# Optimization experiments

Hardware: AMD Instinct MI355X
Metric: run time of the kernel (lower is better)

Reference implementation:

```python
import jax, jax.numpy as jnp
import numpy as np

IN_DIM = 1024
LOW_D_FF = 128
OUT_DIM = 1024
B = 8
S = 2048

def _xavier_normal(key, shape):
    fan_in, fan_out = shape[1], shape[0]
    std = float(np.sqrt(2.0 / (fan_in + fan_out)))
    return jax.random.normal(key, shape, dtype=jnp.float32) * std

def setup_inputs() -> dict:
    key = jax.random.key(0)
    kx, kk, kd, ku = jax.random.split(key, 4)
    x = jax.random.normal(kx, (B, S, IN_DIM), dtype=jnp.float32)
    k = jax.random.normal(kk, (B, LOW_D_FF), dtype=jnp.float32)
    D_matrix = _xavier_normal(kd, (IN_DIM * LOW_D_FF, LOW_D_FF))
    U_matrix = _xavier_normal(ku, (LOW_D_FF * OUT_DIM, LOW_D_FF))
    return {"x": x, "k": k, "D_matrix": D_matrix, "U_matrix": U_matrix}

def reference(x, k, D_matrix, U_matrix):
    # x: [B, S, in_dim], k: [B, low_d_ff]
    Bn = x.shape[0]
    low = k.shape[-1]
    # hypernetwork weight generation: per-sample D [B, in_dim, low], U [B, low, out_dim]
    D = jnp.einsum('pk,bk->bp', D_matrix, k).reshape(Bn, IN_DIM, low)
    U = jnp.einsum('pk,bk->bp', U_matrix, k).reshape(Bn, low, OUT_DIM)
    h = jax.nn.relu(jnp.einsum('bsd,bdl->bsl', x, D))
    return jnp.einsum('bsl,blo->bso', h, U)
```

## Files before the change

### kernel.cpp

```cpp
#include <hip/hip_runtime.h>
#include <hip/hip_bf16.h>
#include <stdint.h>

#define IN_DIM  1024
#define LOW     128
#define OUT_DIM 1024
#define BATCH   8
#define SEQ     2048

typedef unsigned short u16;
typedef short bf16x8 __attribute__((ext_vector_type(8)));
typedef unsigned short u16x4 __attribute__((ext_vector_type(4)));
typedef float f32x4 __attribute__((ext_vector_type(4)));

__device__ __forceinline__ u16 f2bf(float f) {
    union { float f; uint32_t u; } v;
    v.f = f;
    uint32_t u = v.u;
    return (u16)((u + 0x7fffu + ((u >> 16) & 1u)) >> 16);
}

__global__ __launch_bounds__(256) void gen_w(const float* __restrict__ Dm,
                                             const float* __restrict__ Um,
                                             const float* __restrict__ kv,
                                             u16* __restrict__ DgT,
                                             u16* __restrict__ UgT) {
    __shared__ u16 tb[8 * 8 * 32];

    int t = threadIdx.x;
    int bid = blockIdx.x;
    bool isU = bid >= 512;
    int rb = isU ? (bid - 512) : bid;
    const float* src = isU ? Um : Dm;
    u16* outp = isU ? UgT : DgT;
    int NTOT = isU ? 1024 : 128;
    int MTOT = isU ? 128 : 1024;
    int sh = isU ? 7 : 4;
    int m0 = (rb >> sh) * 32;
    int n0 = (rb & ((1 << sh) - 1)) * 8;

    int lane = t & 63, w = t >> 6;
    int lr = lane & 15;
    int hi = lane >> 4;

    bf16x8 bfrag[4];
#pragma unroll
    for (int ks = 0; ks < 4; ++ks)
#pragma unroll
        for (int j = 0; j < 8; ++j) {
            float kvf = (lr < 8) ? kv[lr * LOW + ks * 32 + hi * 8 + j] : 0.f;
            bfrag[ks][j] = (short)f2bf(kvf);
        }

    const float* abase = src +
        ((size_t)(m0 + w * 8 + (lr >> 3)) * NTOT + n0 + (lr & 7)) * 128 + hi * 8;
    size_t tstep = (size_t)2 * NTOT * 128;

#define ISSUE(Lb, tau)                                                        \
    {                                                                         \
        const float* rp = abase + (size_t)(tau) * tstep;                      \
        _Pragma("unroll")                                                     \
        for (int ks = 0; ks < 4; ++ks) {                                      \
            Lb[2 * ks]     = *(const f32x4*)(rp + ks * 32);                   \
            Lb[2 * ks + 1] = *(const f32x4*)(rp + ks * 32 + 4);               \
        }                                                                     \
    }

#define COMPUTE(Lb, tau)                                                      \
    {                                                                         \
        f32x4 acc = (f32x4){0.f, 0.f, 0.f, 0.f};                              \
        _Pragma("unroll")                                                     \
        for (int ks = 0; ks < 4; ++ks) {                                      \
            f32x4 v0 = Lb[2 * ks], v1 = Lb[2 * ks + 1];                       \
            bf16x8 afr;                                                       \
            afr[0] = (short)f2bf(v0.x); afr[1] = (short)f2bf(v0.y);           \
            afr[2] = (short)f2bf(v0.z); afr[3] = (short)f2bf(v0.w);           \
            afr[4] = (short)f2bf(v1.x); afr[5] = (short)f2bf(v1.y);           \
            afr[6] = (short)f2bf(v1.z); afr[7] = (short)f2bf(v1.w);           \
            acc = __builtin_amdgcn_mfma_f32_16x16x32_bf16(afr, bfrag[ks],     \
                                                          acc, 0, 0, 0);      \
        }                                                                     \
        if (lr < 8) {                                                         \
            _Pragma("unroll")                                                 \
            for (int j = 0; j < 4; ++j) {                                     \
                int r = hi * 4 + j;                                           \
                int mm = w * 8 + (tau) * 2 + (r >> 3);                        \
                tb[lr * 256 + (r & 7) * 32 + mm] = f2bf(acc[j]);              \
            }                                                                 \
        }                                                                     \
    }

    f32x4 LA[8], LB[8];
    ISSUE(LA, 0)
    ISSUE(LB, 1)
    COMPUTE(LA, 0)
    ISSUE(LA, 2)
    COMPUTE(LB, 1)
    ISSUE(LB, 3)
    COMPUTE(LA, 2)
    COMPUTE(LB, 3)
#undef ISSUE
#undef COMPUTE

    __syncthreads();

    int c64 = t >> 2, q4 = t & 3;
    int bw = c64 >> 3, np = c64 & 7;
    bf16x8 v = *(const bf16x8*)(tb + bw * 256 + np * 32 + q4 * 8);
    *(bf16x8*)(outp + ((size_t)(bw * NTOT + n0 + np)) * MTOT + m0 + q4 * 8) = v;
}

__global__ __launch_bounds__(256) void fc1(const float* __restrict__ x,
                                           const u16* __restrict__ DgT,
                                           u16* __restrict__ h) {
    __shared__ u16 As[32][72];
    __shared__ u16 Bs[128][72];
    int t = threadIdx.x;
    int bid = blockIdx.x;
    int b = bid >> 6, st = bid & 63;
    int s0 = st * 32;
    const float* xb = x + ((size_t)b * SEQ + s0) * IN_DIM;
    const u16* Db = DgT + (size_t)b * LOW * IN_DIM;

    int w = t >> 6, lane = t & 63;
    int wm = w >> 1, wn = w & 1;
    int lr = lane & 15, hi = lane >> 4;

    f32x4 acc[4];
#pragma unroll
    for (int nf = 0; nf < 4; ++nf) acc[nf] = (f32x4){0.f, 0.f, 0.f, 0.f};

    int ar = t >> 3, ac = t & 7;
    int brt = t >> 3, bc = t & 7;

    for (int kt = 0; kt < IN_DIM / 64; ++kt) {
        int k0 = kt * 64;
#pragma unroll
        for (int i = 0; i < 2; ++i) {
            float4 v = *(const float4*)(xb + (size_t)ar * IN_DIM + k0 + ac * 4 + i * 32);
            u16x4 o;
            o.x = f2bf(v.x); o.y = f2bf(v.y); o.z = f2bf(v.z); o.w = f2bf(v.w);
            *(u16x4*)(&As[ar][ac * 4 + i * 32]) = o;
        }
#pragma unroll
        for (int i = 0; i < 4; ++i) {
            int row = brt + 32 * i;
            bf16x8 v = *(const bf16x8*)(Db + (size_t)row * IN_DIM + k0 + bc * 8);
            *(bf16x8*)(&Bs[row][bc * 8]) = v;
        }
        __syncthreads();
#pragma unroll
        for (int ks = 0; ks < 2; ++ks) {
            int kk = ks * 32 + hi * 8;
            bf16x8 af = *(const bf16x8*)(&As[wm * 16 + lr][kk]);
#pragma unroll
            for (int nf = 0; nf < 4; ++nf) {
                bf16x8 bf = *(const bf16x8*)(&Bs[wn * 64 + nf * 16 + lr][kk]);
                acc[nf] = __builtin_amdgcn_mfma_f32_16x16x32_bf16(af, bf, acc[nf], 0, 0, 0);
            }
        }
        __syncthreads();
    }
    u16* hb = h + ((size_t)b * SEQ + s0) * LOW;
#pragma unroll
    for (int nf = 0; nf < 4; ++nf) {
        int col = wn * 64 + nf * 16 + lr;
#pragma unroll
        for (int j = 0; j < 4; ++j) {
            int rrow = wm * 16 + hi * 4 + j;
            hb[(size_t)rrow * LOW + col] = f2bf(fmaxf(acc[nf][j], 0.f));
        }
    }
}

__global__ __launch_bounds__(256) void fc2(const u16* __restrict__ h,
                                           const u16* __restrict__ UgT,
                                           float* __restrict__ out) {
    __shared__ u16 As[128 * 128];
    __shared__ u16 Bs[128 * 128];
    int t = threadIdx.x;
    int bid = blockIdx.x;
    int b = bid >> 7, st = (bid >> 3) & 15, ot = bid & 7;
    int s0 = st * 128, o0 = ot * 128;
    const u16* hb = h + ((size_t)b * SEQ + s0) * LOW;
    const u16* Ub = UgT + ((size_t)b * OUT_DIM + o0) * LOW;

#pragma unroll
    for (int i = 0; i < 8; ++i) {
        int ch = i * 256 + t;
        int row = ch >> 4, c = ch & 15;
        int swc = c ^ (row & 7);
        *(bf16x8*)(As + row * 128 + swc * 8) = *(const bf16x8*)(hb + (size_t)ch * 8);
        *(bf16x8*)(Bs + row * 128 + swc * 8) = *(const bf16x8*)(Ub + (size_t)ch * 8);
    }
    __syncthreads();

    int w = t >> 6, lane = t & 63;
    int wm = w >> 1, wn = w & 1;
    int lr = lane & 15, lkc = (lane >> 4);

    f32x4 acc[4][4];
#pragma unroll
    for (int mf = 0; mf < 4; ++mf)
#pragma unroll
        for (int nf = 0; nf < 4; ++nf)
            acc[mf][nf] = (f32x4){0.f, 0.f, 0.f, 0.f};

#pragma unroll
    for (int ks = 0; ks < 4; ++ks) {
        bf16x8 af[4], bfr[4];
#pragma unroll
        for (int mf = 0; mf < 4; ++mf) {
            int row = wm * 64 + mf * 16 + lr;
            int swc = (ks * 4 + lkc) ^ (row & 7);
            af[mf] = *(const bf16x8*)(As + row * 128 + swc * 8);
        }
#pragma unroll
        for (int nf = 0; nf < 4; ++nf) {
            int row = wn * 64 + nf * 16 + lr;
            int swc = (ks * 4 + lkc) ^ (row & 7);
            bfr[nf] = *(const bf16x8*)(Bs + row * 128 + swc * 8);
        }
#pragma unroll
        for (int mf = 0; mf < 4; ++mf)
#pragma unroll
            for (int nf = 0; nf < 4; ++nf)
                acc[mf][nf] = __builtin_amdgcn_mfma_f32_16x16x32_bf16(
                    af[mf], bfr[nf], acc[mf][nf], 0, 0, 0);
    }

    float* ob = out + ((size_t)b * SEQ + s0) * OUT_DIM + o0;
#pragma unroll
    for (int mf = 0; mf < 4; ++mf)
#pragma unroll
        for (int nf = 0; nf < 4; ++nf) {
            int col = wn * 64 + nf * 16 + lr;
#pragma unroll
            for (int j = 0; j < 4; ++j) {
                int rrow = wm * 64 + mf * 16 + (lane >> 4) * 4 + j;
                ob[(size_t)rrow * OUT_DIM + col] = acc[mf][nf][j];
            }
        }
}

extern "C" void kernel_launch(void* const* d_in, const int* in_sizes, int n_in,
                              void* d_out, int out_size, void* d_ws, size_t ws_size,
                              hipStream_t stream) {
    const float* x  = (const float*)d_in[0];
    const float* kv = (const float*)d_in[1];
    const float* Dm = (const float*)d_in[2];
    const float* Um = (const float*)d_in[3];
    float* out = (float*)d_out;

    u16* DgT = (u16*)d_ws;
    u16* UgT = DgT + (size_t)BATCH * LOW * IN_DIM;
    u16* hbuf = UgT + (size_t)BATCH * OUT_DIM * LOW;

    gen_w<<<dim3(1024), dim3(256), 0, stream>>>(Dm, Um, kv, DgT, UgT);
    fc1<<<dim3(512), dim3(256), 0, stream>>>(x, DgT, hbuf);
    fc2<<<dim3(1024), dim3(256), 0, stream>>>(hbuf, UgT, out);
}
```

Baseline: 69.51 us.

## Read hypernetwork matrices in contiguous rows and add separate U transpose kernel

gen_w now gives each block 1024 contiguous rows of D_matrix or U_matrix, uses 512 threads and a deeper three-buffer load pipeline, and stages outputs in a padded LDS buffer. D is written transposed directly. U is written untransposed to a scratch buffer and a new transposeU kernel produces the UgT layout. The aim is more streaming-friendly reads of the large fp32 weight matrices, at the cost of an extra kernel launch and an extra round trip of U through global memory.

```diff
diff --git a/kernel.cpp b/kernel.cpp
--- a/kernel.cpp
+++ b/kernel.cpp
@@ -20,24 +20,18 @@
     return (u16)((u + 0x7fffu + ((u >> 16) & 1u)) >> 16);
 }
 
-__global__ __launch_bounds__(256) void gen_w(const float* __restrict__ Dm,
+__global__ __launch_bounds__(512) void gen_w(const float* __restrict__ Dm,
                                              const float* __restrict__ Um,
                                              const float* __restrict__ kv,
                                              u16* __restrict__ DgT,
-                                             u16* __restrict__ UgT) {
-    __shared__ u16 tb[8 * 8 * 32];
+                                             u16* __restrict__ Utmp) {
+    __shared__ u16 tb[8 * 1032];
 
     int t = threadIdx.x;
     int bid = blockIdx.x;
-    bool isU = bid >= 512;
-    int rb = isU ? (bid - 512) : bid;
+    bool isU = bid >= 128;
     const float* src = isU ? Um : Dm;
-    u16* outp = isU ? UgT : DgT;
-    int NTOT = isU ? 1024 : 128;
-    int MTOT = isU ? 128 : 1024;
-    int sh = isU ? 7 : 4;
-    int m0 = (rb >> sh) * 32;
-    int n0 = (rb & ((1 << sh) - 1)) * 8;
+    size_t p0 = (size_t)(isU ? bid - 128 : bid) * 1024;
 
     int lane = t & 63, w = t >> 6;
     int lr = lane & 15;
@@ -52,13 +46,11 @@
             bfrag[ks][j] = (short)f2bf(kvf);
         }
 
-    const float* abase = src +
-        ((size_t)(m0 + w * 8 + (lr >> 3)) * NTOT + n0 + (lr & 7)) * 128 + hi * 8;
-    size_t tstep = (size_t)2 * NTOT * 128;
+    const float* abase = src + (p0 + (size_t)w * 128 + lr) * 128 + hi * 8;
 
 #define ISSUE(Lb, tau)                                                        \
     {                                                                         \
-        const float* rp = abase + (size_t)(tau) * tstep;                      \
+        const float* rp = abase + (size_t)(tau) * 2048;                       \
         _Pragma("unroll")                                                     \
         for (int ks = 0; ks < 4; ++ks) {                                      \
             Lb[2 * ks]     = *(const f32x4*)(rp + ks * 32);                   \
@@ -81,33 +73,78 @@
                                                           acc, 0, 0, 0);      \
         }                                                                     \
         if (lr < 8) {                                                         \
-            _Pragma("unroll")                                                 \
-            for (int j = 0; j < 4; ++j) {                                     \
-                int r = hi * 4 + j;                                           \
-                int mm = w * 8 + (tau) * 2 + (r >> 3);                        \
-                tb[lr * 256 + (r & 7) * 32 + mm] = f2bf(acc[j]);              \
-            }                                                                 \
+            u16x4 o4;                                                         \
+            o4[0] = f2bf(acc[0]); o4[1] = f2bf(acc[1]);                       \
+            o4[2] = f2bf(acc[2]); o4[3] = f2bf(acc[3]);                       \
+            *(u16x4*)(tb + lr * 1032 + w * 128 + (tau) * 16 + hi * 4) = o4;   \
         }                                                                     \
     }
 
-    f32x4 LA[8], LB[8];
-    ISSUE(LA, 0)
-    ISSUE(LB, 1)
-    COMPUTE(LA, 0)
-    ISSUE(LA, 2)
-    COMPUTE(LB, 1)
-    ISSUE(LB, 3)
-    COMPUTE(LA, 2)
-    COMPUTE(LB, 3)
+    f32x4 LA[8], LB[8], LC[8];
+    ISSUE(LA, 0) ISSUE(LB, 1) ISSUE(LC, 2)
+    COMPUTE(LA, 0) ISSUE(LA, 3)
+    COMPUTE(LB, 1) ISSUE(LB, 4)
+    COMPUTE(LC, 2) ISSUE(LC, 5)
+    COMPUTE(LA, 3) ISSUE(LA, 6)
+    COMPUTE(LB, 4) ISSUE(LB, 7)
+    COMPUTE(LC, 5)
+    COMPUTE(LA, 6)
+    COMPUTE(LB, 7)
 #undef ISSUE
 #undef COMPUTE
 
     __syncthreads();
 
-    int c64 = t >> 2, q4 = t & 3;
-    int bw = c64 >> 3, np = c64 & 7;
-    bf16x8 v = *(const bf16x8*)(tb + bw * 256 + np * 32 + q4 * 8);
-    *(bf16x8*)(outp + ((size_t)(bw * NTOT + n0 + np)) * MTOT + m0 + q4 * 8) = v;
+    if (!isU) {
+        int d0 = bid * 8;
+#pragma unroll
+        for (int g = t; g < 1024; g += 512) {
+            int b = g >> 7, l = g & 127;
+            bf16x8 vv;
+#pragma unroll
+            for (int dd = 0; dd < 8; ++dd)
+                vv[dd] = (short)tb[b * 1032 + dd * 128 + l];
+            *(bf16x8*)(DgT + ((size_t)(b * 128 + l) * 1024) + d0) = vv;
+        }
+    } else {
+        int l0 = bid - 128;
+        int b = t >> 6, o0 = (t & 63) * 16;
+        u16* urow = Utmp + ((size_t)l0 * 8 + b) * 1024;
+        bf16x8 v0 = *(const bf16x8*)(tb + b * 1032 + o0);
+        bf16x8 v1 = *(const bf16x8*)(tb + b * 1032 + o0 + 8);
+        *(bf16x8*)(urow + o0) = v0;
+        *(bf16x8*)(urow + o0 + 8) = v1;
+    }
+}
+
+__global__ __launch_bounds__(256) void transposeU(const u16* __restrict__ Utmp,
+                                                  u16* __restrict__ UgT) {
+    __shared__ u16 lds[128 * 72];
+    int t = threadIdx.x;
+    int b = blockIdx.x >> 4, o0 = (blockIdx.x & 15) * 64;
+
+    {
+        int l = t >> 1, half = t & 1;
+        const u16* rp = Utmp + ((size_t)l * 8 + b) * 1024 + o0 + half * 32;
+#pragma unroll
+        for (int i = 0; i < 4; ++i)
+            *(bf16x8*)(lds + l * 72 + half * 32 + i * 8) =
+                *(const bf16x8*)(rp + i * 8);
+    }
+    __syncthreads();
+
+    {
+        int o = t >> 2, q = t & 3;
+        u16* wp = UgT + ((size_t)b * OUT_DIM + o0 + o) * LOW + q * 32;
+#pragma unroll
+        for (int i = 0; i < 4; ++i) {
+            bf16x8 vv;
+#pragma unroll
+            for (int j = 0; j < 8; ++j)
+                vv[j] = (short)lds[(q * 32 + i * 8 + j) * 72 + o];
+            *(bf16x8*)(wp + i * 8) = vv;
+        }
+    }
 }
 
 __global__ __launch_bounds__(256) void fc1(const float* __restrict__ x,
@@ -252,11 +289,13 @@
     const float* Um = (const float*)d_in[3];
     float* out = (float*)d_out;
 
-    u16* DgT = (u16*)d_ws;
-    u16* UgT = DgT + (size_t)BATCH * LOW * IN_DIM;
+    u16* DgT  = (u16*)d_ws;
+    u16* UgT  = DgT + (size_t)BATCH * LOW * IN_DIM;
     u16* hbuf = UgT + (size_t)BATCH * OUT_DIM * LOW;
-
-    gen_w<<<dim3(1024), dim3(256), 0, stream>>>(Dm, Um, kv, DgT, UgT);
+    u16* Utmp = hbuf + (size_t)BATCH * SEQ * LOW;
+
+    gen_w<<<dim3(256), dim3(512), 0, stream>>>(Dm, Um, kv, DgT, Utmp);
+    transposeU<<<dim3(128), dim3(256), 0, stream>>>(Utmp, UgT);
     fc1<<<dim3(512), dim3(256), 0, stream>>>(x, DgT, hbuf);
     fc2<<<dim3(1024), dim3(256), 0, stream>>>(hbuf, UgT, out);
 }
```

Result: slower. 74.42 us (+7.1%).

## Fuse fc1 and fc2 into one kernel keeping h tile in shared memory

Applied to the files above, without the earlier changes.

Merges the two GEMM kernels so each block computes a 32-row relu(xD) tile into LDS, then loops over all 8 output column chunks, loading U tiles and writing the fp32 output directly. This removes the global round trip of the bf16 intermediate h and one kernel launch. The block-to-batch mapping is also interleaved so neighbouring blocks hit different batches. In exchange there are only 512 blocks doing the second GEMM with small 32-row tiles, the U tiles are reloaded per block without double buffering, and LDS use grows.

```diff
diff --git a/kernel.cpp b/kernel.cpp
--- a/kernel.cpp
+++ b/kernel.cpp
@@ -110,14 +110,18 @@
     *(bf16x8*)(outp + ((size_t)(bw * NTOT + n0 + np)) * MTOT + m0 + q4 * 8) = v;
 }
 
-__global__ __launch_bounds__(256) void fc1(const float* __restrict__ x,
-                                           const u16* __restrict__ DgT,
-                                           u16* __restrict__ h) {
+__global__ __launch_bounds__(256) void fc12(const float* __restrict__ x,
+                                            const u16* __restrict__ DgT,
+                                            const u16* __restrict__ UgT,
+                                            float* __restrict__ out) {
     __shared__ u16 As[32][72];
     __shared__ u16 Bs[128][72];
+    __shared__ u16 hs[32 * 128];
+    __shared__ u16 Us[128 * 128];
+
     int t = threadIdx.x;
     int bid = blockIdx.x;
-    int b = bid >> 6, st = bid & 63;
+    int b = bid & 7, st = bid >> 3;
     int s0 = st * 32;
     const float* xb = x + ((size_t)b * SEQ + s0) * IN_DIM;
     const u16* Db = DgT + (size_t)b * LOW * IN_DIM;
@@ -161,86 +165,70 @@
         }
         __syncthreads();
     }
-    u16* hb = h + ((size_t)b * SEQ + s0) * LOW;
 #pragma unroll
     for (int nf = 0; nf < 4; ++nf) {
         int col = wn * 64 + nf * 16 + lr;
+        int c = col >> 3;
 #pragma unroll
         for (int j = 0; j < 4; ++j) {
-            int rrow = wm * 16 + hi * 4 + j;
-            hb[(size_t)rrow * LOW + col] = f2bf(fmaxf(acc[nf][j], 0.f));
-        }
-    }
-}
-
-__global__ __launch_bounds__(256) void fc2(const u16* __restrict__ h,
-                                           const u16* __restrict__ UgT,
-                                           float* __restrict__ out) {
-    __shared__ u16 As[128 * 128];
-    __shared__ u16 Bs[128 * 128];
-    int t = threadIdx.x;
-    int bid = blockIdx.x;
-    int b = bid >> 7, st = (bid >> 3) & 15, ot = bid & 7;
-    int s0 = st * 128, o0 = ot * 128;
-    const u16* hb = h + ((size_t)b * SEQ + s0) * LOW;
-    const u16* Ub = UgT + ((size_t)b * OUT_DIM + o0) * LOW;
-
-#pragma unroll
-    for (int i = 0; i < 8; ++i) {
-        int ch = i * 256 + t;
-        int row = ch >> 4, c = ch & 15;
-        int swc = c ^ (row & 7);
-        *(bf16x8*)(As + row * 128 + swc * 8) = *(const bf16x8*)(hb + (size_t)ch * 8);
-        *(bf16x8*)(Bs + row * 128 + swc * 8) = *(const bf16x8*)(Ub + (size_t)ch * 8);
+            int row = wm * 16 + hi * 4 + j;
+            int swc = c ^ (row & 7);
+            hs[row * 128 + swc * 8 + (col & 7)] = f2bf(fmaxf(acc[nf][j], 0.f));
+        }
     }
     __syncthreads();
 
-    int w = t >> 6, lane = t & 63;
-    int wm = w >> 1, wn = w & 1;
-    int lr = lane & 15, lkc = (lane >> 4);
-
-    f32x4 acc[4][4];
-#pragma unroll
-    for (int mf = 0; mf < 4; ++mf)
-#pragma unroll
-        for (int nf = 0; nf < 4; ++nf)
-            acc[mf][nf] = (f32x4){0.f, 0.f, 0.f, 0.f};
-
-#pragma unroll
-    for (int ks = 0; ks < 4; ++ks) {
-        bf16x8 af[4], bfr[4];
-#pragma unroll
-        for (int mf = 0; mf < 4; ++mf) {
-            int row = wm * 64 + mf * 16 + lr;
-            int swc = (ks * 4 + lkc) ^ (row & 7);
-            af[mf] = *(const bf16x8*)(As + row * 128 + swc * 8);
-        }
+    bf16x8 ah[4];
+    {
+        int row = wm * 16 + lr;
+#pragma unroll
+        for (int ks = 0; ks < 4; ++ks) {
+            int swc = (ks * 4 + hi) ^ (row & 7);
+            ah[ks] = *(const bf16x8*)(hs + row * 128 + swc * 8);
+        }
+    }
+
+    const u16* Ub = UgT + (size_t)b * OUT_DIM * LOW;
+    float* ob = out + ((size_t)b * SEQ + s0) * OUT_DIM;
+
+    for (int oc = 0; oc < 8; ++oc) {
+#pragma unroll
+        for (int i = 0; i < 8; ++i) {
+            int ch = i * 256 + t;
+            int row = ch >> 4, c = ch & 15;
+            int swc = c ^ (row & 7);
+            *(bf16x8*)(Us + row * 128 + swc * 8) =
+                *(const bf16x8*)(Ub + (size_t)(oc * 128 + row) * 128 + c * 8);
+        }
+        __syncthreads();
+
+        f32x4 acc2[4];
+#pragma unroll
+        for (int nf = 0; nf < 4; ++nf) acc2[nf] = (f32x4){0.f, 0.f, 0.f, 0.f};
+
+#pragma unroll
+        for (int ks = 0; ks < 4; ++ks) {
+#pragma unroll
+            for (int nf = 0; nf < 4; ++nf) {
+                int row = wn * 64 + nf * 16 + lr;
+                int swc = (ks * 4 + hi) ^ (row & 7);
+                bf16x8 bfr = *(const bf16x8*)(Us + row * 128 + swc * 8);
+                acc2[nf] = __builtin_amdgcn_mfma_f32_16x16x32_bf16(
+                    ah[ks], bfr, acc2[nf], 0, 0, 0);
+            }
+        }
+
 #pragma unroll
         for (int nf = 0; nf < 4; ++nf) {
-            int row = wn * 64 + nf * 16 + lr;
-            int swc = (ks * 4 + lkc) ^ (row & 7);
-            bfr[nf] = *(const bf16x8*)(Bs + row * 128 + swc * 8);
-        }
-#pragma unroll
-        for (int mf = 0; mf < 4; ++mf)
-#pragma unroll
-            for (int nf = 0; nf < 4; ++nf)
-                acc[mf][nf] = __builtin_amdgcn_mfma_f32_16x16x32_bf16(
-                    af[mf], bfr[nf], acc[mf][nf], 0, 0, 0);
-    }
-
-    float* ob = out + ((size_t)b * SEQ + s0) * OUT_DIM + o0;
-#pragma unroll
-    for (int mf = 0; mf < 4; ++mf)
-#pragma unroll
-        for (int nf = 0; nf < 4; ++nf) {
-            int col = wn * 64 + nf * 16 + lr;
+            int col = oc * 128 + wn * 64 + nf * 16 + lr;
 #pragma unroll
             for (int j = 0; j < 4; ++j) {
-                int rrow = wm * 64 + mf * 16 + (lane >> 4) * 4 + j;
-                ob[(size_t)rrow * OUT_DIM + col] = acc[mf][nf][j];
+                int row = wm * 16 + hi * 4 + j;
+                ob[(size_t)row * OUT_DIM + col] = acc2[nf][j];
             }
         }
+        __syncthreads();
+    }
 }
 
 extern "C" void kernel_launch(void* const* d_in, const int* in_sizes, int n_in,
@@ -252,11 +240,9 @@
     const float* Um = (const float*)d_in[3];
     float* out = (float*)d_out;
 
-    u16* DgT = (u16*)d_ws;
-    u16* UgT = DgT + (size_t)BATCH * LOW * IN_DIM;
-    u16* hbuf = UgT + (size_t)BATCH * OUT_DIM * LOW;
+    u16* DgT  = (u16*)d_ws;
+    u16* UgT  = DgT + (size_t)BATCH * LOW * IN_DIM;
 
     gen_w<<<dim3(1024), dim3(256), 0, stream>>>(Dm, Um, kv, DgT, UgT);
-    fc1<<<dim3(512), dim3(256), 0, stream>>>(x, DgT, hbuf);
-    fc2<<<dim3(1024), dim3(256), 0, stream>>>(hbuf, UgT, out);
-}
+    fc12<<<dim3(512), dim3(256), 0, stream>>>(x, DgT, UgT, out);
+}
```

New measurement: 63.44 us. 8.7% less time.
